# Performance work log

Hardware: AMD Instinct MI355X
Metric: run time of the kernel (lower is better)

## Reference

```python
import jax, jax.numpy as jnp
import numpy as np

N = 100_000      # nodes
E = 3_200_000    # edges (avg degree 32)
F_IN = 100       # raw feature dim (embedding Linear(100, 64))
H = 64           # in/hidden/out channels
C = 18           # class_num
EPS = 1e-12      # F.normalize eps


def _sage_conv(x, src, dst, edge_weight, Wl, bl, Wr):
    """PyG-style SAGEConv: mean-aggregate neighbor messages, two linears, L2 normalize."""
    msg = x[src]                                   # [E, d] gather of x_j
    if edge_weight is not None:
        msg = msg * edge_weight[:, None]
    agg = jax.ops.segment_sum(msg, dst, num_segments=N)                       # [N, d]
    deg = jax.ops.segment_sum(jnp.ones((src.shape[0],), x.dtype), dst, num_segments=N)
    mean = agg / jnp.maximum(deg, 1.0)[:, None]
    out = mean @ Wl + bl + x @ Wr                  # lin_l(aggr) + lin_r(root)
    nrm = jnp.sqrt(jnp.sum(out * out, axis=-1, keepdims=True))
    return out / jnp.maximum(nrm, EPS)


def setup_inputs() -> dict:
    key = jax.random.key(0)
    ks = jax.random.split(key, 16)
    s = 0.1
    inp = {
        "x": jax.random.normal(ks[0], (N, F_IN), jnp.float32),
        "edge_index": jax.random.randint(ks[1], (2, E), 0, N, dtype=jnp.int64),
        "edge_weight": jax.random.uniform(ks[2], (E,), jnp.float32),
        "emb_W": jax.random.normal(ks[3], (F_IN, H), jnp.float32) * s,
        "emb_b": jnp.zeros((H,), jnp.float32),
    }
    k = 4
    for i in (1, 2, 3):
        inp[f"Wl{i}"] = jax.random.normal(ks[k], (H, H), jnp.float32) * s; k += 1
        inp[f"bl{i}"] = jnp.zeros((H,), jnp.float32)
        inp[f"Wr{i}"] = jax.random.normal(ks[k], (H, H), jnp.float32) * s; k += 1
    inp["Wl4"] = jax.random.normal(ks[k], (H, C), jnp.float32) * s; k += 1
    inp["bl4"] = jnp.zeros((C,), jnp.float32)
    inp["Wr4"] = jax.random.normal(ks[k], (H, C), jnp.float32) * s
    return inp


def reference(x, edge_index, edge_weight, emb_W, emb_b,
              Wl1, bl1, Wr1, Wl2, bl2, Wr2, Wl3, bl3, Wr3,
              Wl4, bl4, Wr4):
    src, dst = edge_index[0], edge_index[1]
    h = jax.nn.relu(x @ emb_W + emb_b)             # embedding MLP
    for Wl, bl, Wr in ((Wl1, bl1, Wr1), (Wl2, bl2, Wr2), (Wl3, bl3, Wr3)):
        h = jax.nn.relu(_sage_conv(h, src, dst, edge_weight, Wl, bl, Wr))
        # dropout p=0.2 is identity in eval mode
    return _sage_conv(h, src, dst, None, Wl4, bl4, Wr4)
```

## Files before the change

kernel.cpp:

```cpp
#include <hip/hip_runtime.h>
#include <hip/hip_bf16.h>

#define N_NODES   100000
#define N_EDGES   3200000
#define F_IN      100
#define H_DIM     64
#define C_NUM     18
#define NPB       256
#define N_BKT     391
#define EPB       8192
#define N_TILES   1563

typedef __attribute__((ext_vector_type(8))) short short8;
typedef __attribute__((ext_vector_type(4))) float f32x4;
typedef __attribute__((ext_vector_type(2))) float f32x2;

#define PLANE_SZ ((size_t)N_NODES * 32)

__device__ __forceinline__ float ldf(const void* p, long long i, int isbf) {
    if (isbf) return __bfloat162float(((const __hip_bfloat16*)p)[i]);
    return ((const float*)p)[i];
}
__device__ __forceinline__ int ldi(const void* p, long long i, int is64) {
    if (is64) return (int)(((const long long*)p)[i]);
    return ((const int*)p)[i];
}
__device__ __forceinline__ unsigned short f2us(float f) {
    __hip_bfloat16 b = __float2bfloat16(f);
    return *(unsigned short*)&b;
}
__device__ __forceinline__ unsigned char f2fp8(float f) {
    int p = __builtin_amdgcn_cvt_pk_fp8_f32(f, 0.0f, 0, false);
    return (unsigned char)(p & 0xFF);
}

__global__ void detect_kernel(const void* ei, const void* x, int* flags)
{
    if (threadIdx.x != 0 || blockIdx.x != 0) return;
    const long long* e64 = (const long long*)ei;
    int ok64 = 1;
    for (int i = 0; i < 128; ++i) {
        long long v = e64[i];
        if (v < 0 || v >= N_NODES) { ok64 = 0; break; }
    }
    const __hip_bfloat16* xb = (const __hip_bfloat16*)x;
    int cnt = 0;
    for (int i = 0; i < 256; ++i) {
        float v = fabsf(__bfloat162float(xb[i]));
        if (v == 0.0f || (v > 9.5367431640625e-7f && v < 1.0e6f)) ++cnt;
    }
    flags[0] = ok64;
    flags[1] = (cnt >= 240) ? 1 : 0;
}

__global__ void zero_cnt(int* __restrict__ pcnt)
{
    int i = threadIdx.x;
    if (i < N_BKT) pcnt[i] = 0;
}

__global__ __launch_bounds__(1024) void radix_count(const void* ei, int* __restrict__ pcnt,
                                                    const int* __restrict__ flags)
{
    __shared__ int hist[N_BKT];
    const int t = threadIdx.x;
    if (t < N_BKT) hist[t] = 0;
    __syncthreads();
    const int base = blockIdx.x * EPB;
    const int n = min(EPB, N_EDGES - base);
    const int is64 = flags[0];
    for (int j = t; j < n; j += 1024) {
        int d = ldi(ei, (long long)N_EDGES + base + j, is64);
        atomicAdd(&hist[d >> 8], 1);
    }
    __syncthreads();
    if (t < N_BKT) atomicAdd(&pcnt[t], hist[t]);
}

__global__ void scan_bkt(const int* __restrict__ cnt, int* __restrict__ base,
                         int* __restrict__ cursor)
{
    __shared__ int tmp[512];
    const int t = threadIdx.x;
    int v = (t < N_BKT) ? cnt[t] : 0;
    tmp[t] = v;
    __syncthreads();
    for (int off = 1; off < 512; off <<= 1) {
        int add = (t >= off) ? tmp[t - off] : 0;
        __syncthreads();
        tmp[t] += add;
        __syncthreads();
    }
    if (t < N_BKT) { base[t] = tmp[t] - v; cursor[t] = tmp[t] - v; }
    if (t == 511) base[N_BKT] = tmp[511];
}

__global__ __launch_bounds__(1024) void radix_scatter(const void* ei, const void* ew,
                                                      int* __restrict__ gcursor,
                                                      uint2* __restrict__ temp,
                                                      const int* __restrict__ flags)
{
    __shared__ uint2 stage[EPB];
    __shared__ int hist[512], scan_s[512];
    __shared__ int gbase[N_BKT], lcur[N_BKT];
    const int t = threadIdx.x;
    if (t < 512) hist[t] = 0;
    __syncthreads();

    const int base = blockIdx.x * EPB;
    const int n = min(EPB, N_EDGES - base);
    const int is64 = flags[0], isbf = flags[1];

    int  bkt[8];
    uint2 pk[8];
#pragma unroll
    for (int j = 0; j < 8; ++j) {
        int i = j * 1024 + t;
        bkt[j] = -1;
        if (i < n) {
            int e = base + i;
            int s = ldi(ei, e, is64);
            int d = ldi(ei, (long long)N_EDGES + e, is64);
            float w = ldf(ew, e, isbf);
            bkt[j] = d >> 8;
            pk[j].x = (unsigned)s | ((unsigned)(d & (NPB - 1)) << 17);
            pk[j].y = (unsigned)f2us(w) | ((unsigned)bkt[j] << 16);
            atomicAdd(&hist[bkt[j]], 1);
        }
    }
    __syncthreads();
    if (t < 512) scan_s[t] = hist[t];
    __syncthreads();
    for (int off = 1; off < 512; off <<= 1) {
        int add = 0;
        if (t < 512 && t >= off) add = scan_s[t - off];
        __syncthreads();
        if (t < 512) scan_s[t] += add;
        __syncthreads();
    }
    if (t < N_BKT) {
        int excl = scan_s[t] - hist[t];
        lcur[t] = excl;
        gbase[t] = atomicAdd(&gcursor[t], hist[t]) - excl;
    }
    __syncthreads();
#pragma unroll
    for (int j = 0; j < 8; ++j) {
        if (bkt[j] >= 0) {
            int pos = atomicAdd(&lcur[bkt[j]], 1);
            stage[pos] = pk[j];
        }
    }
    __syncthreads();
#pragma unroll
    for (int j = 0; j < 8; ++j) {
        int i = j * 1024 + t;
        if (i < n) {
            int b = (int)(stage[i].y >> 16);
            temp[gbase[b] + i] = stage[i];
        }
    }
}

__global__ __launch_bounds__(256) void csr_build(const uint2* __restrict__ temp,
                          const int* __restrict__ pbase,
                          unsigned int* __restrict__ csr_pk,
                          int* __restrict__ deg, int* __restrict__ row_start,
                          float* __restrict__ inv_deg)
{
    __shared__ int cnt[NPB], scan_s[NPB], cur[NPB];
    const int b = blockIdx.x;
    const int t = threadIdx.x;
    cnt[t] = 0;
    __syncthreads();
    const int bs = pbase[b];
    const int be = pbase[b + 1];
    for (int i = bs + t; i < be; i += NPB)
        atomicAdd(&cnt[(temp[i].x >> 17) & (NPB - 1)], 1);
    __syncthreads();
    int v = cnt[t];
    scan_s[t] = v;
    __syncthreads();
    for (int off = 1; off < NPB; off <<= 1) {
        int add = (t >= off) ? scan_s[t - off] : 0;
        __syncthreads();
        scan_s[t] += add;
        __syncthreads();
    }
    int excl = bs + scan_s[t] - v;
    cur[t] = excl;
    int node = b * NPB + t;
    if (node < N_NODES) {
        deg[node]       = v;
        row_start[node] = excl;
        inv_deg[node]   = 1.0f / (float)max(v, 1);
    }
    __syncthreads();
    for (int i = bs + t; i < be; i += NPB) {
        uint2 e = temp[i];
        int k = (e.x >> 17) & (NPB - 1);
        int pos = atomicAdd(&cur[k], 1);
        csr_pk[pos] = (e.x & 0x1FFFFu) | ((e.y & 0x7FFFu) << 17);
    }
}

template <int CP, int COUT>
__device__ __forceinline__ void stage_W(unsigned short* W_s, const void* Wl, const void* Wr,
                                        int t, int isbf)
{
    constexpr int KP = 136;
    const int n0 = t >> 3, k8a = t & 7;
    for (int n = n0; n < CP; n += 32) {
#pragma unroll
        for (int hh = 0; hh < 2; ++hh) {
            int k8 = k8a + hh * 8;
            union { unsigned short u[8]; short8 v; } tmp;
#pragma unroll
            for (int j = 0; j < 8; ++j) {
                int k = k8 * 8 + j;
                float val = 0.0f;
                if (n < COUT && k < 128)
                    val = (k < 64) ? ldf(Wl, (long long)k * COUT + n, isbf)
                                   : ldf(Wr, (long long)(k - 64) * COUT + n, isbf);
                tmp.u[j] = f2us(val);
            }
            *(short8*)&W_s[n * KP + k8 * 8] = tmp.v;
        }
    }
}

__global__ void embed_mfma(const void* x, const void* W, const void* b,
                           __hip_bfloat16* __restrict__ h,
                           unsigned char* __restrict__ h8,
                           const int* __restrict__ flags)
{
    constexpr int KP = 136;
    __shared__ unsigned short W_s[H_DIM * KP];
    __shared__ unsigned short x_s[64 * KP];
    __shared__ float b_s[H_DIM];
    const int t = threadIdx.x;
    const int isbf = flags[1];

    {
        const int n0 = t >> 3, k8a = t & 7;
        for (int n = n0; n < H_DIM; n += 32) {
#pragma unroll
            for (int hh = 0; hh < 2; ++hh) {
                int k8 = k8a + hh * 8;
                union { unsigned short u[8]; short8 v; } tmp;
#pragma unroll
                for (int j = 0; j < 8; ++j) {
                    int k = k8 * 8 + j;
                    tmp.u[j] = (k < F_IN) ? f2us(ldf(W, (long long)k * H_DIM + n, isbf))
                                          : (unsigned short)0;
                }
                *(short8*)&W_s[n * KP + k8 * 8] = tmp.v;
            }
        }
    }
    if (t < H_DIM) b_s[t] = ldf(b, t, isbf);
    for (int i = t; i < 64 * 36; i += 256) {
        int row = i / 36, col = 100 + (i % 36);
        x_s[row * KP + col] = 0;
    }

    const int wave = t >> 6, lane = t & 63, c = lane & 15, quad = lane >> 4;

    for (int tile = blockIdx.x; tile < N_TILES; tile += gridDim.x) {
        const int nb0 = tile * 64;
        const int valid = min(64, N_NODES - nb0);
        __syncthreads();
        if (isbf) {
            const uint2* xu = (const uint2*)x + (size_t)nb0 * 25;
            for (int i2 = t; i2 < valid * 25; i2 += 256) {
                int row = i2 / 25, col4 = i2 - row * 25;
                *(uint2*)&x_s[row * KP + col4 * 4] = xu[i2];
            }
        } else {
            for (int i = t; i < valid * 100; i += 256) {
                int row = i / 100, col = i - row * 100;
                x_s[row * KP + col] = f2us(((const float*)x)[(size_t)(nb0 + row) * 100 + col]);
            }
        }
        if (valid < 64) {
            for (int i = t; i < (64 - valid) * 100; i += 256) {
                int row = valid + i / 100, col = i % 100;
                x_s[row * KP + col] = 0;
            }
        }
        __syncthreads();

        short8 bfrag[4][4];
#pragma unroll
        for (int nt = 0; nt < 4; ++nt)
#pragma unroll
            for (int kt = 0; kt < 4; ++kt)
                bfrag[nt][kt] = *(const short8*)&W_s[(nt * 16 + c) * KP + kt * 32 + quad * 8];

        short8 afrag[4];
#pragma unroll
        for (int kt = 0; kt < 4; ++kt)
            afrag[kt] = *(const short8*)&x_s[(wave * 16 + c) * KP + kt * 32 + quad * 8];

        f32x4 acc[4] = {};
#pragma unroll
        for (int nt = 0; nt < 4; ++nt)
#pragma unroll
            for (int kt = 0; kt < 4; ++kt)
                acc[nt] = __builtin_amdgcn_mfma_f32_16x16x32_bf16(afrag[kt], bfrag[nt][kt], acc[nt], 0, 0, 0);

        const int nb = nb0 + wave * 16;
#pragma unroll
        for (int nt = 0; nt < 4; ++nt)
#pragma unroll
            for (int reg = 0; reg < 4; ++reg) {
                int nn = nb + quad * 4 + reg;
                int col = nt * 16 + c;
                if (nn < N_NODES) {
                    float v = fmaxf(acc[nt][reg] + b_s[col], 0.0f);
                    h[(size_t)nn * H_DIM + col] = __float2bfloat16(v);
                    h8[(size_t)(col >> 5) * PLANE_SZ + (size_t)nn * 32 + (col & 31)] = f2fp8(v);
                }
            }
    }
}

#define ACC16(HV, W) do {                                                          \
    f32x2 f_;                                                                      \
    f_ = __builtin_amdgcn_cvt_pk_f32_fp8((int)HV.x, false); a[0]=fmaf(W,f_.x,a[0]);  a[1]=fmaf(W,f_.y,a[1]);   \
    f_ = __builtin_amdgcn_cvt_pk_f32_fp8((int)HV.x, true ); a[2]=fmaf(W,f_.x,a[2]);  a[3]=fmaf(W,f_.y,a[3]);   \
    f_ = __builtin_amdgcn_cvt_pk_f32_fp8((int)HV.y, false); a[4]=fmaf(W,f_.x,a[4]);  a[5]=fmaf(W,f_.y,a[5]);   \
    f_ = __builtin_amdgcn_cvt_pk_f32_fp8((int)HV.y, true ); a[6]=fmaf(W,f_.x,a[6]);  a[7]=fmaf(W,f_.y,a[7]);   \
    f_ = __builtin_amdgcn_cvt_pk_f32_fp8((int)HV.z, false); a[8]=fmaf(W,f_.x,a[8]);  a[9]=fmaf(W,f_.y,a[9]);   \
    f_ = __builtin_amdgcn_cvt_pk_f32_fp8((int)HV.z, true ); a[10]=fmaf(W,f_.x,a[10]); a[11]=fmaf(W,f_.y,a[11]); \
    f_ = __builtin_amdgcn_cvt_pk_f32_fp8((int)HV.w, false); a[12]=fmaf(W,f_.x,a[12]); a[13]=fmaf(W,f_.y,a[13]); \
    f_ = __builtin_amdgcn_cvt_pk_f32_fp8((int)HV.w, true ); a[14]=fmaf(W,f_.x,a[14]); a[15]=fmaf(W,f_.y,a[15]); \
} while (0)

template <bool USE_W>
__global__ __launch_bounds__(256) void gather_mean(const unsigned char* __restrict__ h8,
                            const unsigned int* __restrict__ csr_pk,
                            const int* __restrict__ row_start,
                            const int* __restrict__ deg,
                            const float* __restrict__ inv_deg,
                            __hip_bfloat16* __restrict__ mean)
{
    const int lane = threadIdx.x & 63;
    const int c2 = lane & 1;
    const int r2 = lane >> 1;
    const int bid = blockIdx.x;
    const int plane = (bid >> 2) & 1;
    const int pb = ((bid >> 3) << 2) | (bid & 3);
    const int wid = pb * 4 + (threadIdx.x >> 6);
    const int nw  = (gridDim.x >> 1) * 4;
    const unsigned char* hp = h8 + (size_t)plane * PLANE_SZ;

    for (int n = wid; n < N_NODES; n += nw) {
        const int s0 = row_start[n];
        const int d0 = deg[n];
        unsigned int ev = (lane < d0) ? csr_pk[s0 + lane] : 0u;
        const int m0 = min(d0, 64);
        float a[16] = {};

        for (int j0 = 0; j0 < m0; j0 += 32) {
            unsigned int e = __shfl(ev, j0 + r2);
            uint4 hv = *(const uint4*)(hp + (size_t)(e & 0x1FFFF) * 32 + 16 * c2);
            float w;
            if (USE_W) w = __uint_as_float((e & 0xFFFE0000u) >> 1);
            else       w = (j0 + r2 < m0) ? 1.0f : 0.0f;
            ACC16(hv, w);
        }
        for (int jb = 64; jb < d0; jb += 32) {
            int j = jb + r2;
            unsigned int e2 = (j < d0) ? csr_pk[s0 + j] : 0u;
            float w;
            if (USE_W) w = __uint_as_float((e2 & 0xFFFE0000u) >> 1);
            else       w = (j < d0) ? 1.0f : 0.0f;
            uint4 hv = *(const uint4*)(hp + (size_t)(e2 & 0x1FFFF) * 32 + 16 * c2);
            ACC16(hv, w);
        }

#pragma unroll
        for (int i = 0; i < 8; ++i) {
            float keep = (lane & 2) ? a[i + 8] : a[i];
            float give = (lane & 2) ? a[i] : a[i + 8];
            a[i] = keep + __shfl_xor(give, 2);
        }
#pragma unroll
        for (int i = 0; i < 4; ++i) {
            float keep = (lane & 4) ? a[i + 4] : a[i];
            float give = (lane & 4) ? a[i] : a[i + 4];
            a[i] = keep + __shfl_xor(give, 4);
        }
#pragma unroll
        for (int i = 0; i < 2; ++i) {
            float keep = (lane & 8) ? a[i + 2] : a[i];
            float give = (lane & 8) ? a[i] : a[i + 2];
            a[i] = keep + __shfl_xor(give, 8);
        }
        {
            float keep = (lane & 16) ? a[1] : a[0];
            float give = (lane & 16) ? a[0] : a[1];
            a[0] = keep + __shfl_xor(give, 16);
        }
        a[0] += __shfl_xor(a[0], 32);

        if (!(lane & 32)) {
            const int f = c2 * 16 + ((lane >> 1) & 1) * 8 + ((lane >> 2) & 1) * 4
                        + ((lane >> 3) & 1) * 2 + ((lane >> 4) & 1);
            mean[(size_t)n * H_DIM + plane * 32 + f] = __float2bfloat16(a[0] * inv_deg[n]);
        }
    }
}

template <int COUT, bool RELU, bool FINAL>
__global__ void transform_mfma(const __hip_bfloat16* __restrict__ meanp,
                               const __hip_bfloat16* __restrict__ hp,
                               const void* Wl, const void* bl, const void* Wr,
                               __hip_bfloat16* __restrict__ h_out,
                               unsigned char* __restrict__ h8_out,
                               const int* __restrict__ flags, void* dout)
{
    constexpr int CP = (COUT + 15) & ~15;
    constexpr int NT = CP / 16;
    constexpr int KP = 136;
    __shared__ unsigned short W_s[CP * KP];
    __shared__ float b_s[CP];
    const int t = threadIdx.x;
    const int isbf = flags[1];
    stage_W<CP, COUT>(W_s, Wl, Wr, t, isbf);
    if (t < CP) b_s[t] = (t < COUT) ? ldf(bl, t, isbf) : 0.0f;
    __syncthreads();

    const int wave = t >> 6, lane = t & 63, c = lane & 15, quad = lane >> 4;
    short8 bfrag[NT][4];
#pragma unroll
    for (int nt = 0; nt < NT; ++nt)
#pragma unroll
        for (int kt = 0; kt < 4; ++kt)
            bfrag[nt][kt] = *(const short8*)&W_s[(nt * 16 + c) * KP + kt * 32 + quad * 8];

    for (int tile = blockIdx.x; tile < N_TILES; tile += gridDim.x) {
        const int nbw = tile * 64 + wave * 16;
        if (nbw >= N_NODES) continue;
        int node = nbw + c; if (node >= N_NODES) node = N_NODES - 1;

        short8 afrag[4];
#pragma unroll
        for (int kt = 0; kt < 4; ++kt) {
            const __hip_bfloat16* sp = (kt < 2) ? meanp : hp;
            afrag[kt] = *(const short8*)(sp + (size_t)node * H_DIM + (kt & 1) * 32 + quad * 8);
        }

        f32x4 acc[NT] = {};
#pragma unroll
        for (int nt = 0; nt < NT; ++nt)
#pragma unroll
            for (int kt = 0; kt < 4; ++kt)
                acc[nt] = __builtin_amdgcn_mfma_f32_16x16x32_bf16(afrag[kt], bfrag[nt][kt], acc[nt], 0, 0, 0);

        float rs[4];
#pragma unroll
        for (int reg = 0; reg < 4; ++reg) {
            float s2 = 0.f;
#pragma unroll
            for (int nt = 0; nt < NT; ++nt) {
                float v = acc[nt][reg] + b_s[nt * 16 + c];
                acc[nt][reg] = v;
                s2 += v * v;
            }
            s2 += __shfl_xor(s2, 1); s2 += __shfl_xor(s2, 2);
            s2 += __shfl_xor(s2, 4); s2 += __shfl_xor(s2, 8);
            rs[reg] = 1.0f / fmaxf(sqrtf(s2), 1e-12f);
        }

#pragma unroll
        for (int nt = 0; nt < NT; ++nt)
#pragma unroll
            for (int reg = 0; reg < 4; ++reg) {
                int nn  = nbw + quad * 4 + reg;
                int col = nt * 16 + c;
                if (nn < N_NODES && col < COUT) {
                    float v = acc[nt][reg] * rs[reg];
                    if (RELU) v = fmaxf(v, 0.0f);
                    if (FINAL) {
                        if (isbf) ((__hip_bfloat16*)dout)[(size_t)nn * COUT + col] = __float2bfloat16(v);
                        else      ((float*)dout)[(size_t)nn * COUT + col] = v;
                    } else {
                        h_out[(size_t)nn * H_DIM + col] = __float2bfloat16(v);
                        h8_out[(size_t)(col >> 5) * PLANE_SZ + (size_t)nn * 32 + (col & 31)] = f2fp8(v);
                    }
                }
            }
    }
}

extern "C" void kernel_launch(void* const* d_in, const int* in_sizes, int n_in,
                              void* d_out, int out_size, void* d_ws, size_t ws_size,
                              hipStream_t stream)
{
    const void* x    = d_in[0];
    const void* ei   = d_in[1];
    const void* ew   = d_in[2];
    const void* embW = d_in[3];
    const void* embB = d_in[4];
    const void* Wl1 = d_in[5];  const void* bl1 = d_in[6];  const void* Wr1 = d_in[7];
    const void* Wl2 = d_in[8];  const void* bl2 = d_in[9];  const void* Wr2 = d_in[10];
    const void* Wl3 = d_in[11]; const void* bl3 = d_in[12]; const void* Wr3 = d_in[13];
    const void* Wl4 = d_in[14]; const void* bl4 = d_in[15]; const void* Wr4 = d_in[16];
    (void)in_sizes; (void)n_in; (void)out_size; (void)ws_size;

    char* ws = (char*)d_ws;
    size_t off = 0;
    auto alloc = [&](size_t bytes) -> void* {
        void* p = ws + off;
        off += (bytes + 255) & ~(size_t)255;
        return p;
    };
    uint2* temp = (uint2*)alloc((size_t)N_EDGES * sizeof(uint2));
    __hip_bfloat16* hA = (__hip_bfloat16*)temp;
    __hip_bfloat16* hB = (__hip_bfloat16*)((char*)temp + (size_t)N_NODES * H_DIM * 2);
    unsigned int* csr_pk = (unsigned int*)alloc((size_t)N_EDGES * sizeof(unsigned int));
    __hip_bfloat16* mn = (__hip_bfloat16*)alloc((size_t)N_NODES * H_DIM * 2);
    unsigned char* h8 = (unsigned char*)alloc((size_t)N_NODES * H_DIM);
    int*   pcnt    = (int*)  alloc((N_BKT)     * sizeof(int));
    int*   pbase   = (int*)  alloc((N_BKT + 1) * sizeof(int));
    int*   pcursor = (int*)  alloc((N_BKT)     * sizeof(int));
    int*   deg     = (int*)  alloc((size_t)N_NODES * sizeof(int));
    int*   row_st  = (int*)  alloc((size_t)N_NODES * sizeof(int));
    float* inv_deg = (float*)alloc((size_t)N_NODES * sizeof(float));
    int*   flags   = (int*)  alloc(256);

    const int NBr = (N_EDGES + EPB - 1) / EPB;

    detect_kernel<<<1, 64, 0, stream>>>(ei, x, flags);
    zero_cnt<<<1, 512, 0, stream>>>(pcnt);
    radix_count<<<NBr, 1024, 0, stream>>>(ei, pcnt, flags);
    scan_bkt<<<1, 512, 0, stream>>>(pcnt, pbase, pcursor);
    radix_scatter<<<NBr, 1024, 0, stream>>>(ei, ew, pcursor, temp, flags);
    csr_build<<<N_BKT, NPB, 0, stream>>>(temp, pbase, csr_pk, deg, row_st, inv_deg);

    embed_mfma<<<512, 256, 0, stream>>>(x, embW, embB, hA, h8, flags);

    gather_mean<true><<<2048, 256, 0, stream>>>(h8, csr_pk, row_st, deg, inv_deg, mn);
    transform_mfma<H_DIM, true, false><<<512, 256, 0, stream>>>(
        mn, hA, Wl1, bl1, Wr1, hB, h8, flags, d_out);
    gather_mean<true><<<2048, 256, 0, stream>>>(h8, csr_pk, row_st, deg, inv_deg, mn);
    transform_mfma<H_DIM, true, false><<<512, 256, 0, stream>>>(
        mn, hB, Wl2, bl2, Wr2, hA, h8, flags, d_out);
    gather_mean<true><<<2048, 256, 0, stream>>>(h8, csr_pk, row_st, deg, inv_deg, mn);
    transform_mfma<H_DIM, true, false><<<512, 256, 0, stream>>>(
        mn, hA, Wl3, bl3, Wr3, hB, h8, flags, d_out);
    gather_mean<false><<<2048, 256, 0, stream>>>(h8, csr_pk, row_st, deg, inv_deg, mn);
    transform_mfma<C_NUM, false, true><<<512, 256, 0, stream>>>(
        mn, hB, Wl4, bl4, Wr4, nullptr, nullptr, flags, d_out);
}
```

Before: 565.4 us.

## Use row-major fp8 features with one-feature-per-lane gather instead of split planes

Drops the two 32-column fp8 plane layout and stores fp8 features row-major with 64 bytes per node. The gather kernel now gives each wave one node and each lane one feature, loading 8 edge indices at a time (uniform across the wave) and doing a byte load per lane, which removes the cross-lane shuffle reduction and the plane-split block mapping. The trade is byte-granular loads and scalar edge reads in place of 16-byte vector loads spread over 32 edges in parallel, so each wave walks the edges of a node one after another and memory-level parallelism per wave drops.

```diff
diff --git a/kernel.cpp b/kernel.cpp
--- a/kernel.cpp
+++ b/kernel.cpp
@@ -14,8 +14,6 @@
 typedef __attribute__((ext_vector_type(8))) short short8;
 typedef __attribute__((ext_vector_type(4))) float f32x4;
 typedef __attribute__((ext_vector_type(2))) float f32x2;
-
-#define PLANE_SZ ((size_t)N_NODES * 32)
 
 __device__ __forceinline__ float ldf(const void* p, long long i, int isbf) {
     if (isbf) return __bfloat162float(((const __hip_bfloat16*)p)[i]);
@@ -319,23 +317,11 @@
                 if (nn < N_NODES) {
                     float v = fmaxf(acc[nt][reg] + b_s[col], 0.0f);
                     h[(size_t)nn * H_DIM + col] = __float2bfloat16(v);
-                    h8[(size_t)(col >> 5) * PLANE_SZ + (size_t)nn * 32 + (col & 31)] = f2fp8(v);
+                    h8[(size_t)nn * H_DIM + col] = f2fp8(v);
                 }
             }
     }
 }
-
-#define ACC16(HV, W) do {                                                          \
-    f32x2 f_;                                                                      \
-    f_ = __builtin_amdgcn_cvt_pk_f32_fp8((int)HV.x, false); a[0]=fmaf(W,f_.x,a[0]);  a[1]=fmaf(W,f_.y,a[1]);   \
-    f_ = __builtin_amdgcn_cvt_pk_f32_fp8((int)HV.x, true ); a[2]=fmaf(W,f_.x,a[2]);  a[3]=fmaf(W,f_.y,a[3]);   \
-    f_ = __builtin_amdgcn_cvt_pk_f32_fp8((int)HV.y, false); a[4]=fmaf(W,f_.x,a[4]);  a[5]=fmaf(W,f_.y,a[5]);   \
-    f_ = __builtin_amdgcn_cvt_pk_f32_fp8((int)HV.y, true ); a[6]=fmaf(W,f_.x,a[6]);  a[7]=fmaf(W,f_.y,a[7]);   \
-    f_ = __builtin_amdgcn_cvt_pk_f32_fp8((int)HV.z, false); a[8]=fmaf(W,f_.x,a[8]);  a[9]=fmaf(W,f_.y,a[9]);   \
-    f_ = __builtin_amdgcn_cvt_pk_f32_fp8((int)HV.z, true ); a[10]=fmaf(W,f_.x,a[10]); a[11]=fmaf(W,f_.y,a[11]); \
-    f_ = __builtin_amdgcn_cvt_pk_f32_fp8((int)HV.w, false); a[12]=fmaf(W,f_.x,a[12]); a[13]=fmaf(W,f_.y,a[13]); \
-    f_ = __builtin_amdgcn_cvt_pk_f32_fp8((int)HV.w, true ); a[14]=fmaf(W,f_.x,a[14]); a[15]=fmaf(W,f_.y,a[15]); \
-} while (0)
 
 template <bool USE_W>
 __global__ __launch_bounds__(256) void gather_mean(const unsigned char* __restrict__ h8,
@@ -346,70 +332,37 @@
                             __hip_bfloat16* __restrict__ mean)
 {
     const int lane = threadIdx.x & 63;
-    const int c2 = lane & 1;
-    const int r2 = lane >> 1;
-    const int bid = blockIdx.x;
-    const int plane = (bid >> 2) & 1;
-    const int pb = ((bid >> 3) << 2) | (bid & 3);
-    const int wid = pb * 4 + (threadIdx.x >> 6);
-    const int nw  = (gridDim.x >> 1) * 4;
-    const unsigned char* hp = h8 + (size_t)plane * PLANE_SZ;
+    const int wid = __builtin_amdgcn_readfirstlane(blockIdx.x * 4 + (threadIdx.x >> 6));
+    const int nw  = gridDim.x * 4;
 
     for (int n = wid; n < N_NODES; n += nw) {
         const int s0 = row_start[n];
         const int d0 = deg[n];
-        unsigned int ev = (lane < d0) ? csr_pk[s0 + lane] : 0u;
-        const int m0 = min(d0, 64);
-        float a[16] = {};
-
-        for (int j0 = 0; j0 < m0; j0 += 32) {
-            unsigned int e = __shfl(ev, j0 + r2);
-            uint4 hv = *(const uint4*)(hp + (size_t)(e & 0x1FFFF) * 32 + 16 * c2);
-            float w;
-            if (USE_W) w = __uint_as_float((e & 0xFFFE0000u) >> 1);
-            else       w = (j0 + r2 < m0) ? 1.0f : 0.0f;
-            ACC16(hv, w);
-        }
-        for (int jb = 64; jb < d0; jb += 32) {
-            int j = jb + r2;
-            unsigned int e2 = (j < d0) ? csr_pk[s0 + j] : 0u;
-            float w;
-            if (USE_W) w = __uint_as_float((e2 & 0xFFFE0000u) >> 1);
-            else       w = (j < d0) ? 1.0f : 0.0f;
-            uint4 hv = *(const uint4*)(hp + (size_t)(e2 & 0x1FFFF) * 32 + 16 * c2);
-            ACC16(hv, w);
-        }
-
-#pragma unroll
-        for (int i = 0; i < 8; ++i) {
-            float keep = (lane & 2) ? a[i + 8] : a[i];
-            float give = (lane & 2) ? a[i] : a[i + 8];
-            a[i] = keep + __shfl_xor(give, 2);
-        }
-#pragma unroll
-        for (int i = 0; i < 4; ++i) {
-            float keep = (lane & 4) ? a[i + 4] : a[i];
-            float give = (lane & 4) ? a[i] : a[i + 4];
-            a[i] = keep + __shfl_xor(give, 4);
-        }
-#pragma unroll
-        for (int i = 0; i < 2; ++i) {
-            float keep = (lane & 8) ? a[i + 2] : a[i];
-            float give = (lane & 8) ? a[i] : a[i + 2];
-            a[i] = keep + __shfl_xor(give, 8);
-        }
-        {
-            float keep = (lane & 16) ? a[1] : a[0];
-            float give = (lane & 16) ? a[0] : a[1];
-            a[0] = keep + __shfl_xor(give, 16);
-        }
-        a[0] += __shfl_xor(a[0], 32);
-
-        if (!(lane & 32)) {
-            const int f = c2 * 16 + ((lane >> 1) & 1) * 8 + ((lane >> 2) & 1) * 4
-                        + ((lane >> 3) & 1) * 2 + ((lane >> 4) & 1);
-            mean[(size_t)n * H_DIM + plane * 32 + f] = __float2bfloat16(a[0] * inv_deg[n]);
-        }
+        float acc = 0.0f;
+        int j = 0;
+        for (; j + 8 <= d0; j += 8) {
+            unsigned int e[8];
+#pragma unroll
+            for (int k = 0; k < 8; ++k) e[k] = csr_pk[s0 + j + k];
+            unsigned int v[8];
+#pragma unroll
+            for (int k = 0; k < 8; ++k)
+                v[k] = h8[(size_t)(e[k] & 0x1FFFFu) * H_DIM + lane];
+#pragma unroll
+            for (int k = 0; k < 8; ++k) {
+                float w = USE_W ? __uint_as_float((e[k] & 0xFFFE0000u) >> 1) : 1.0f;
+                f32x2 p = __builtin_amdgcn_cvt_pk_f32_fp8((int)v[k], false);
+                acc = fmaf(w, p.x, acc);
+            }
+        }
+        for (; j < d0; ++j) {
+            unsigned int e = csr_pk[s0 + j];
+            unsigned int v = h8[(size_t)(e & 0x1FFFFu) * H_DIM + lane];
+            float w = USE_W ? __uint_as_float((e & 0xFFFE0000u) >> 1) : 1.0f;
+            f32x2 p = __builtin_amdgcn_cvt_pk_f32_fp8((int)v, false);
+            acc = fmaf(w, p.x, acc);
+        }
+        mean[(size_t)n * H_DIM + lane] = __float2bfloat16(acc * inv_deg[n]);
     }
 }
 
@@ -488,7 +441,7 @@
                         else      ((float*)dout)[(size_t)nn * COUT + col] = v;
                     } else {
                         h_out[(size_t)nn * H_DIM + col] = __float2bfloat16(v);
-                        h8_out[(size_t)(col >> 5) * PLANE_SZ + (size_t)nn * 32 + (col & 31)] = f2fp8(v);
+                        h8_out[(size_t)nn * H_DIM + col] = f2fp8(v);
                     }
                 }
             }
```

Result: no change. 571.5 us (+1.1%).
